# Performance work log

Measured on AMD Instinct MI355X. Metric: run time of the kernel, lower is better.

The kernel has to match this reference:

```python
import jax, jax.numpy as jnp
import numpy as np


def _conv1x1(x, w, b):
    # x: [B, Cin, H, W]; w: [Cout, Cin, 1, 1]; b: [Cout]
    y = jnp.einsum('bchw,oc->bohw', x, w[:, :, 0, 0])
    return y + b[None, :, None, None]


def setup_inputs() -> dict:
    key = jax.random.key(0)
    ks = jax.random.split(key, 9)
    B, C, H, W = 8, 256, 64, 64
    Cq = C // 4
    sc = 0.05
    return {
        'x': jax.random.normal(ks[0], (B, C, H, W), jnp.float32),
        'query_weight': jax.random.normal(ks[1], (Cq, C, 1, 1), jnp.float32) * sc,
        'query_bias': jax.random.normal(ks[2], (Cq,), jnp.float32) * sc,
        'key_weight': jax.random.normal(ks[3], (Cq, C, 1, 1), jnp.float32) * sc,
        'key_bias': jax.random.normal(ks[4], (Cq,), jnp.float32) * sc,
        'value_weight': jax.random.normal(ks[5], (C, C, 1, 1), jnp.float32) * sc,
        'value_bias': jax.random.normal(ks[6], (C,), jnp.float32) * sc,
        'gamma_weight': jax.random.normal(ks[7], (C, C, 1, 1), jnp.float32) * sc,
        'gamma_bias': jax.random.normal(ks[8], (C,), jnp.float32) * sc,
    }


def reference(x, query_weight, query_bias, key_weight, key_bias,
              value_weight, value_bias, gamma_weight, gamma_bias):
    B, C, H, W = x.shape
    N = H * W
    q = _conv1x1(x, query_weight, query_bias).reshape(B, -1, N)   # [B, Cq, N]
    k = _conv1x1(x, key_weight, key_bias).reshape(B, -1, N)       # [B, Cq, N]
    v = _conv1x1(x, value_weight, value_bias).reshape(B, C, N)    # [B, C, N]
    # energy[b, i, j] = sum_c q[b, c, i] * k[b, c, j]
    energy = jnp.einsum('bci,bcj->bij', q, k)                     # [B, N, N]
    energy = jax.nn.elu(energy) / N
    out = jnp.einsum('bcn,bnm->bcm', v, energy).reshape(B, C, H, W)
    return _conv1x1(out, gamma_weight, gamma_bias)
```

## Files before the change

### kernel.cpp

```cpp
#include <hip/hip_runtime.h>
#include <cmath>

#define BB 8
#define CC 256
#define CQ 64
#define NN 4096
constexpr float INV_N = 1.0f / 4096.0f;

typedef __attribute__((ext_vector_type(8))) short short8;
typedef __attribute__((ext_vector_type(4))) short short4v;
typedef __attribute__((ext_vector_type(4))) float float4v;

__device__ __forceinline__ short f2bf(float f) {
  union { float f; unsigned u; } x; x.f = f;
  unsigned r = x.u + 0x7fffu + ((x.u >> 16) & 1u);
  return (short)(r >> 16);
}

__global__ void wconv_kernel(const float* __restrict__ wq,
                             const float* __restrict__ wk,
                             const float* __restrict__ wv,
                             const float* __restrict__ wg,
                             short* __restrict__ wqb, short* __restrict__ wkb,
                             short* __restrict__ wvb, short* __restrict__ wgb) {
  const int t = blockIdx.x * 256 + threadIdx.x;
  const float* src;
  short* dst;
  int idx;
  if (t < 4096)        { src = wq; dst = wqb; idx = t; }
  else if (t < 8192)   { src = wk; dst = wkb; idx = t - 4096; }
  else if (t < 24576)  { src = wv; dst = wvb; idx = t - 8192; }
  else                 { src = wg; dst = wgb; idx = t - 24576; }
  const float4 v = *reinterpret_cast<const float4*>(&src[(size_t)idx * 4]);
  short4v o;
  o[0] = f2bf(v.x); o[1] = f2bf(v.y); o[2] = f2bf(v.z); o[3] = f2bf(v.w);
  *reinterpret_cast<short4v*>(&dst[(size_t)idx * 4]) = o;
}

__global__ __launch_bounds__(256, 2) void qkv_kernel(
    const float* __restrict__ X,
    const short* __restrict__ wqb, const float* __restrict__ bq,
    const short* __restrict__ wkb, const float* __restrict__ bk,
    const short* __restrict__ wvb, const float* __restrict__ bv,
    short* __restrict__ qt, short* __restrict__ kt, short* __restrict__ vbf) {
  __shared__ short xt[64 * 272];
  __shared__ short Os[64 * 72];
  const int tid = threadIdx.x;
  const int wid = tid >> 6;
  const int lane = tid & 63, quad = lane >> 4, l16 = lane & 15;
  const int b = blockIdx.x, n0 = blockIdx.y * 64;

#pragma unroll 4
  for (int p = 0; p < 16; ++p) {
    const int idx = p * 256 + tid;
    const int c = idx >> 4;
    const int n4 = (idx & 15) * 4;
    const float4 x4 = *reinterpret_cast<const float4*>(
        &X[((size_t)b * CC + c) * NN + n0 + n4]);
    xt[(n4 + 0) * 272 + c] = f2bf(x4.x);
    xt[(n4 + 1) * 272 + c] = f2bf(x4.y);
    xt[(n4 + 2) * 272 + c] = f2bf(x4.z);
    xt[(n4 + 3) * 272 + c] = f2bf(x4.w);
  }
  __syncthreads();

  for (int ch = 0; ch < 6; ++ch) {
    const short* W; const float* bias; int obase;
    if (ch == 0)      { W = wqb; bias = bq; obase = 0; }
    else if (ch == 1) { W = wkb; bias = bk; obase = 0; }
    else { W = wvb + (size_t)(ch - 2) * 64 * CC; bias = bv + (ch - 2) * 64; obase = (ch - 2) * 64; }

    float4v acc[4];
#pragma unroll
    for (int tm = 0; tm < 4; ++tm) acc[tm] = float4v{0.f, 0.f, 0.f, 0.f};

    const short* wrow = &W[(size_t)(wid * 16 + l16) * CC + quad * 8];
    short8 a_cur = *reinterpret_cast<const short8*>(wrow);
#pragma unroll
    for (int kk = 0; kk < 8; ++kk) {
      short8 a_nxt = a_cur;
      if (kk < 7) a_nxt = *reinterpret_cast<const short8*>(wrow + (kk + 1) * 32);
#pragma unroll
      for (int tm = 0; tm < 4; ++tm) {
        const short8 bfrag = *reinterpret_cast<const short8*>(
            &xt[(tm * 16 + l16) * 272 + kk * 32 + quad * 8]);
        acc[tm] = __builtin_amdgcn_mfma_f32_16x16x32_bf16(a_cur, bfrag, acc[tm], 0, 0, 0);
      }
      a_cur = a_nxt;
    }

    if (ch < 2) {
      short* dst = (ch == 0) ? qt : kt;
#pragma unroll
      for (int tm = 0; tm < 4; ++tm) {
        short4v pk;
#pragma unroll
        for (int r = 0; r < 4; ++r)
          pk[r] = f2bf(acc[tm][r] + bias[wid * 16 + quad * 4 + r]);
        *reinterpret_cast<short4v*>(
            &dst[((size_t)b * NN + n0 + tm * 16 + l16) * 64 + wid * 16 + quad * 4]) = pk;
      }
    } else {
      __syncthreads();
#pragma unroll
      for (int tm = 0; tm < 4; ++tm)
#pragma unroll
        for (int r = 0; r < 4; ++r)
          Os[(wid * 16 + quad * 4 + r) * 72 + tm * 16 + l16] =
              f2bf(acc[tm][r] + bias[wid * 16 + quad * 4 + r]);
      __syncthreads();
      const int o = tid >> 2, ng = (tid & 3) * 16;
      const short8 s0 = *reinterpret_cast<const short8*>(&Os[o * 72 + ng]);
      const short8 s1 = *reinterpret_cast<const short8*>(&Os[o * 72 + ng + 8]);
      short* vp = &vbf[((size_t)b * CC + obase + o) * NN + n0 + ng];
      *reinterpret_cast<short8*>(vp) = s0;
      *reinterpret_cast<short8*>(vp + 8) = s1;
    }
  }
}

__global__ __launch_bounds__(256, 2) void attn_kernel(
    const short* __restrict__ qt, const short* __restrict__ kt,
    const short* __restrict__ vbf, const short* __restrict__ wgb,
    const float* __restrict__ bg, float* __restrict__ out) {
  __shared__ short smem[16896];
  short* Es0 = smem;
  short* Es1 = smem + 4608;
  short* Outs = smem;

  const int tid = threadIdx.x;
  const int wid = tid >> 6;
  const int lane = tid & 63, quad = lane >> 4, l16 = lane & 15;
  const int b = blockIdx.x, m0 = blockIdx.y * 64;

  short8 bkf[4][2];
#pragma unroll
  for (int tm = 0; tm < 4; ++tm)
#pragma unroll
    for (int kk = 0; kk < 2; ++kk)
      bkf[tm][kk] = *reinterpret_cast<const short8*>(
          &kt[((size_t)b * NN + m0 + tm * 16 + l16) * 64 + kk * 32 + quad * 8]);

  const short* qrow = &qt[((size_t)b * NN + wid * 16 + l16) * 64 + quad * 8];
  const short* vrow[4];
#pragma unroll
  for (int tc = 0; tc < 4; ++tc)
    vrow[tc] = &vbf[((size_t)b * CC + wid * 64 + tc * 16 + l16) * NN + quad * 8];

  float4v acc[4][4];
#pragma unroll
  for (int i = 0; i < 4; ++i)
#pragma unroll
    for (int j = 0; j < 4; ++j) acc[i][j] = float4v{0.f, 0.f, 0.f, 0.f};

  short8 aq0 = *reinterpret_cast<const short8*>(qrow);
  short8 aq1 = *reinterpret_cast<const short8*>(qrow + 32);
  short8 av0[4][2], av1[4][2];
#pragma unroll
  for (int tc = 0; tc < 4; ++tc) {
    av0[tc][0] = *reinterpret_cast<const short8*>(vrow[tc]);
    av0[tc][1] = *reinterpret_cast<const short8*>(vrow[tc] + 32);
  }

  auto body = [&](int it, short8 (&avc)[4][2], short8 (&avn)[4][2]) {
    short* Esw = (it & 1) ? Es1 : Es0;
    const int nbn = (it + 1) * 64;

#pragma unroll
    for (int tc = 0; tc < 4; ++tc) {
      avn[tc][0] = *reinterpret_cast<const short8*>(vrow[tc] + nbn);
      avn[tc][1] = *reinterpret_cast<const short8*>(vrow[tc] + nbn + 32);
    }

    float4v s[4];
#pragma unroll
    for (int tm = 0; tm < 4; ++tm) {
      float4v t = {0.f, 0.f, 0.f, 0.f};
      t = __builtin_amdgcn_mfma_f32_16x16x32_bf16(aq0, bkf[tm][0], t, 0, 0, 0);
      t = __builtin_amdgcn_mfma_f32_16x16x32_bf16(aq1, bkf[tm][1], t, 0, 0, 0);
      s[tm] = t;
    }

    const short8 aq0n = *reinterpret_cast<const short8*>(qrow + (size_t)nbn * 64);
    const short8 aq1n = *reinterpret_cast<const short8*>(qrow + (size_t)nbn * 64 + 32);

#pragma unroll
    for (int tm = 0; tm < 4; ++tm) {
      short4v pk;
#pragma unroll
      for (int r = 0; r < 4; ++r) {
        float sv = s[tm][r];
        sv = (sv > 0.f) ? sv : (__expf(sv) - 1.f);
        pk[r] = f2bf(sv * INV_N);
      }
      *reinterpret_cast<short4v*>(
          &Esw[(tm * 16 + l16) * 72 + wid * 16 + quad * 4]) = pk;
    }
    __syncthreads();

#pragma unroll
    for (int tm = 0; tm < 4; ++tm) {
      const short8 be0 = *reinterpret_cast<const short8*>(
          &Esw[(tm * 16 + l16) * 72 + quad * 8]);
      const short8 be1 = *reinterpret_cast<const short8*>(
          &Esw[(tm * 16 + l16) * 72 + 32 + quad * 8]);
#pragma unroll
      for (int tc = 0; tc < 4; ++tc) {
        acc[tc][tm] = __builtin_amdgcn_mfma_f32_16x16x32_bf16(avc[tc][0], be0, acc[tc][tm], 0, 0, 0);
        acc[tc][tm] = __builtin_amdgcn_mfma_f32_16x16x32_bf16(avc[tc][1], be1, acc[tc][tm], 0, 0, 0);
      }
    }
    aq0 = aq0n; aq1 = aq1n;
  };

  for (int it = 0; it < 64; it += 2) {
    body(it, av0, av1);
    body(it + 1, av1, av0);
  }

  __syncthreads();
#pragma unroll
  for (int tc = 0; tc < 4; ++tc)
#pragma unroll
    for (int tm = 0; tm < 4; ++tm) {
      short4v pk;
#pragma unroll
      for (int r = 0; r < 4; ++r) pk[r] = f2bf(acc[tc][tm][r]);
      *reinterpret_cast<short4v*>(
          &Outs[(tm * 16 + l16) * 264 + wid * 64 + tc * 16 + quad * 4]) = pk;
    }
  __syncthreads();

#pragma unroll
  for (int i = 0; i < 4; ++i)
#pragma unroll
    for (int j = 0; j < 4; ++j) acc[i][j] = float4v{0.f, 0.f, 0.f, 0.f};

  for (int ks8 = 0; ks8 < 8; ++ks8) {
    short8 ag[4];
#pragma unroll
    for (int to = 0; to < 4; ++to)
      ag[to] = *reinterpret_cast<const short8*>(
          &wgb[(size_t)(wid * 64 + to * 16 + l16) * CC + ks8 * 32 + quad * 8]);
    short8 bo[4];
#pragma unroll
    for (int tm = 0; tm < 4; ++tm)
      bo[tm] = *reinterpret_cast<const short8*>(
          &Outs[(tm * 16 + l16) * 264 + ks8 * 32 + quad * 8]);
#pragma unroll
    for (int to = 0; to < 4; ++to)
#pragma unroll
      for (int tm = 0; tm < 4; ++tm)
        acc[to][tm] =
            __builtin_amdgcn_mfma_f32_16x16x32_bf16(ag[to], bo[tm], acc[to][tm], 0, 0, 0);
  }

#pragma unroll
  for (int to = 0; to < 4; ++to) {
#pragma unroll
    for (int r = 0; r < 4; ++r) {
      const int o = wid * 64 + to * 16 + quad * 4 + r;
      const float bgv = bg[o];
#pragma unroll
      for (int tm = 0; tm < 4; ++tm) {
        out[((size_t)b * CC + o) * NN + m0 + tm * 16 + l16] =
            acc[to][tm][r] + bgv;
      }
    }
  }
}

extern "C" void kernel_launch(void* const* d_in, const int* in_sizes, int n_in,
                              void* d_out, int out_size, void* d_ws,
                              size_t ws_size, hipStream_t stream) {
  const float* x  = (const float*)d_in[0];
  const float* wq = (const float*)d_in[1];
  const float* bq = (const float*)d_in[2];
  const float* wk = (const float*)d_in[3];
  const float* bk = (const float*)d_in[4];
  const float* wv = (const float*)d_in[5];
  const float* bv = (const float*)d_in[6];
  const float* wg = (const float*)d_in[7];
  const float* bg = (const float*)d_in[8];
  float* out = (float*)d_out;

  short* qt  = (short*)d_ws;
  short* kt  = qt + (size_t)BB * NN * CQ;
  short* vbf = kt + (size_t)BB * NN * CQ;
  short* wqb = vbf + (size_t)BB * CC * NN;
  short* wkb = wqb + (size_t)CQ * CC;
  short* wvb = wkb + (size_t)CQ * CC;
  short* wgb = wvb + (size_t)CC * CC;

  wconv_kernel<<<dim3(160), 256, 0, stream>>>(wq, wk, wv, wg, wqb, wkb, wvb, wgb);
  qkv_kernel<<<dim3(BB, NN / 64), 256, 0, stream>>>(x, wqb, bq, wkb, bk, wvb, bv,
                                                    qt, kt, vbf);
  attn_kernel<<<dim3(BB, NN / 64), 256, 0, stream>>>(qt, kt, vbf, wgb, bg, out);
}
```

Measured before the change: 271.2 us.

## Halve spatial tile to 32 in QKV and attention kernels, raise occupancy

After: 419.5 us. 54.7% more time.

```diff
diff --git a/kernel.cpp b/kernel.cpp
--- a/kernel.cpp
+++ b/kernel.cpp
@@ -37,24 +37,24 @@
   *reinterpret_cast<short4v*>(&dst[(size_t)idx * 4]) = o;
 }
 
-__global__ __launch_bounds__(256, 2) void qkv_kernel(
+__global__ __launch_bounds__(256, 4) void qkv_kernel(
     const float* __restrict__ X,
     const short* __restrict__ wqb, const float* __restrict__ bq,
     const short* __restrict__ wkb, const float* __restrict__ bk,
     const short* __restrict__ wvb, const float* __restrict__ bv,
     short* __restrict__ qt, short* __restrict__ kt, short* __restrict__ vbf) {
-  __shared__ short xt[64 * 272];
-  __shared__ short Os[64 * 72];
+  __shared__ short xt[32 * 272];
+  __shared__ short Os[64 * 40];
   const int tid = threadIdx.x;
   const int wid = tid >> 6;
   const int lane = tid & 63, quad = lane >> 4, l16 = lane & 15;
-  const int b = blockIdx.x, n0 = blockIdx.y * 64;
+  const int b = blockIdx.x, n0 = blockIdx.y * 32;
 
 #pragma unroll 4
-  for (int p = 0; p < 16; ++p) {
+  for (int p = 0; p < 8; ++p) {
     const int idx = p * 256 + tid;
-    const int c = idx >> 4;
-    const int n4 = (idx & 15) * 4;
+    const int c = idx >> 3;
+    const int n4 = (idx & 7) * 4;
     const float4 x4 = *reinterpret_cast<const float4*>(
         &X[((size_t)b * CC + c) * NN + n0 + n4]);
     xt[(n4 + 0) * 272 + c] = f2bf(x4.x);
@@ -70,9 +70,9 @@
     else if (ch == 1) { W = wkb; bias = bk; obase = 0; }
     else { W = wvb + (size_t)(ch - 2) * 64 * CC; bias = bv + (ch - 2) * 64; obase = (ch - 2) * 64; }
 
-    float4v acc[4];
-#pragma unroll
-    for (int tm = 0; tm < 4; ++tm) acc[tm] = float4v{0.f, 0.f, 0.f, 0.f};
+    float4v acc[2];
+#pragma unroll
+    for (int tm = 0; tm < 2; ++tm) acc[tm] = float4v{0.f, 0.f, 0.f, 0.f};
 
     const short* wrow = &W[(size_t)(wid * 16 + l16) * CC + quad * 8];
     short8 a_cur = *reinterpret_cast<const short8*>(wrow);
@@ -81,7 +81,7 @@
       short8 a_nxt = a_cur;
       if (kk < 7) a_nxt = *reinterpret_cast<const short8*>(wrow + (kk + 1) * 32);
 #pragma unroll
-      for (int tm = 0; tm < 4; ++tm) {
+      for (int tm = 0; tm < 2; ++tm) {
         const short8 bfrag = *reinterpret_cast<const short8*>(
             &xt[(tm * 16 + l16) * 272 + kk * 32 + quad * 8]);
         acc[tm] = __builtin_amdgcn_mfma_f32_16x16x32_bf16(a_cur, bfrag, acc[tm], 0, 0, 0);
@@ -92,7 +92,7 @@
     if (ch < 2) {
       short* dst = (ch == 0) ? qt : kt;
 #pragma unroll
-      for (int tm = 0; tm < 4; ++tm) {
+      for (int tm = 0; tm < 2; ++tm) {
         short4v pk;
 #pragma unroll
         for (int r = 0; r < 4; ++r)
@@ -103,95 +103,86 @@
     } else {
       __syncthreads();
 #pragma unroll
-      for (int tm = 0; tm < 4; ++tm)
+      for (int tm = 0; tm < 2; ++tm)
 #pragma unroll
         for (int r = 0; r < 4; ++r)
-          Os[(wid * 16 + quad * 4 + r) * 72 + tm * 16 + l16] =
+          Os[(wid * 16 + quad * 4 + r) * 40 + tm * 16 + l16] =
               f2bf(acc[tm][r] + bias[wid * 16 + quad * 4 + r]);
       __syncthreads();
-      const int o = tid >> 2, ng = (tid & 3) * 16;
-      const short8 s0 = *reinterpret_cast<const short8*>(&Os[o * 72 + ng]);
-      const short8 s1 = *reinterpret_cast<const short8*>(&Os[o * 72 + ng + 8]);
+      const int o = tid >> 2, ng = (tid & 3) * 8;
+      const short8 s0 = *reinterpret_cast<const short8*>(&Os[o * 40 + ng]);
       short* vp = &vbf[((size_t)b * CC + obase + o) * NN + n0 + ng];
       *reinterpret_cast<short8*>(vp) = s0;
-      *reinterpret_cast<short8*>(vp + 8) = s1;
-    }
-  }
-}
-
-__global__ __launch_bounds__(256, 2) void attn_kernel(
+    }
+  }
+}
+
+__global__ __launch_bounds__(256, 4) void attn_kernel(
     const short* __restrict__ qt, const short* __restrict__ kt,
     const short* __restrict__ vbf, const short* __restrict__ wgb,
     const float* __restrict__ bg, float* __restrict__ out) {
-  __shared__ short smem[16896];
+  __shared__ short smem[8448];
   short* Es0 = smem;
-  short* Es1 = smem + 4608;
+  short* Es1 = smem + 2304;
   short* Outs = smem;
 
   const int tid = threadIdx.x;
   const int wid = tid >> 6;
   const int lane = tid & 63, quad = lane >> 4, l16 = lane & 15;
-  const int b = blockIdx.x, m0 = blockIdx.y * 64;
-
-  short8 bkf[4][2];
-#pragma unroll
-  for (int tm = 0; tm < 4; ++tm)
+  const int b = blockIdx.x, m0 = blockIdx.y * 32;
+
+  short8 bkf[2][2];
+#pragma unroll
+  for (int tm = 0; tm < 2; ++tm)
 #pragma unroll
     for (int kk = 0; kk < 2; ++kk)
       bkf[tm][kk] = *reinterpret_cast<const short8*>(
           &kt[((size_t)b * NN + m0 + tm * 16 + l16) * 64 + kk * 32 + quad * 8]);
 
-  const short* qrow = &qt[((size_t)b * NN + wid * 16 + l16) * 64 + quad * 8];
-  const short* vrow[4];
-#pragma unroll
-  for (int tc = 0; tc < 4; ++tc)
-    vrow[tc] = &vbf[((size_t)b * CC + wid * 64 + tc * 16 + l16) * NN + quad * 8];
-
-  float4v acc[4][4];
+  const short* qp = &qt[((size_t)b * NN + wid * 16 + l16) * 64 + quad * 8];
+  const short* vp0 = &vbf[((size_t)b * CC + wid * 64 +  0 + l16) * NN + quad * 8];
+  const short* vp1 = &vbf[((size_t)b * CC + wid * 64 + 16 + l16) * NN + quad * 8];
+  const short* vp2 = &vbf[((size_t)b * CC + wid * 64 + 32 + l16) * NN + quad * 8];
+  const short* vp3 = &vbf[((size_t)b * CC + wid * 64 + 48 + l16) * NN + quad * 8];
+
+  float4v acc[4][2];
 #pragma unroll
   for (int i = 0; i < 4; ++i)
 #pragma unroll
-    for (int j = 0; j < 4; ++j) acc[i][j] = float4v{0.f, 0.f, 0.f, 0.f};
-
-  short8 aq0 = *reinterpret_cast<const short8*>(qrow);
-  short8 aq1 = *reinterpret_cast<const short8*>(qrow + 32);
-  short8 av0[4][2], av1[4][2];
-#pragma unroll
-  for (int tc = 0; tc < 4; ++tc) {
-    av0[tc][0] = *reinterpret_cast<const short8*>(vrow[tc]);
-    av0[tc][1] = *reinterpret_cast<const short8*>(vrow[tc] + 32);
-  }
-
-  auto body = [&](int it, short8 (&avc)[4][2], short8 (&avn)[4][2]) {
+    for (int j = 0; j < 2; ++j) acc[i][j] = float4v{0.f, 0.f, 0.f, 0.f};
+
+  for (int it = 0; it < 64; ++it) {
     short* Esw = (it & 1) ? Es1 : Es0;
-    const int nbn = (it + 1) * 64;
-
-#pragma unroll
-    for (int tc = 0; tc < 4; ++tc) {
-      avn[tc][0] = *reinterpret_cast<const short8*>(vrow[tc] + nbn);
-      avn[tc][1] = *reinterpret_cast<const short8*>(vrow[tc] + nbn + 32);
-    }
-
-    float4v s[4];
-#pragma unroll
-    for (int tm = 0; tm < 4; ++tm) {
+
+    short8 av[4][2];
+    av[0][0] = *reinterpret_cast<const short8*>(vp0);
+    av[0][1] = *reinterpret_cast<const short8*>(vp0 + 32);
+    av[1][0] = *reinterpret_cast<const short8*>(vp1);
+    av[1][1] = *reinterpret_cast<const short8*>(vp1 + 32);
+    av[2][0] = *reinterpret_cast<const short8*>(vp2);
+    av[2][1] = *reinterpret_cast<const short8*>(vp2 + 32);
+    av[3][0] = *reinterpret_cast<const short8*>(vp3);
+    av[3][1] = *reinterpret_cast<const short8*>(vp3 + 32);
+    const short8 aq0 = *reinterpret_cast<const short8*>(qp);
+    const short8 aq1 = *reinterpret_cast<const short8*>(qp + 32);
+
+    float4v s[2];
+#pragma unroll
+    for (int tm = 0; tm < 2; ++tm) {
       float4v t = {0.f, 0.f, 0.f, 0.f};
       t = __builtin_amdgcn_mfma_f32_16x16x32_bf16(aq0, bkf[tm][0], t, 0, 0, 0);
       t = __builtin_amdgcn_mfma_f32_16x16x32_bf16(aq1, bkf[tm][1], t, 0, 0, 0);
       s[tm] = t;
     }
 
-    const short8 aq0n = *reinterpret_cast<const short8*>(qrow + (size_t)nbn * 64);
-    const short8 aq1n = *reinterpret_cast<const short8*>(qrow + (size_t)nbn * 64 + 32);
-
-#pragma unroll
-    for (int tm = 0; tm < 4; ++tm) {
+#pragma unroll
+    for (int tm = 0; tm < 2; ++tm) {
       short4v pk;
 #pragma unroll
       for (int r = 0; r < 4; ++r) {
         float sv = s[tm][r];
         sv = (sv > 0.f) ? sv : (__expf(sv) - 1.f);
-        pk[r] = f2bf(sv * INV_N);
+        pk[r] = f2bf(sv);
       }
       *reinterpret_cast<short4v*>(
           &Esw[(tm * 16 + l16) * 72 + wid * 16 + quad * 4]) = pk;
@@ -199,33 +190,33 @@
     __syncthreads();
 
 #pragma unroll
-    for (int tm = 0; tm < 4; ++tm) {
+    for (int tm = 0; tm < 2; ++tm) {
       const short8 be0 = *reinterpret_cast<const short8*>(
           &Esw[(tm * 16 + l16) * 72 + quad * 8]);
       const short8 be1 = *reinterpret_cast<const short8*>(
           &Esw[(tm * 16 + l16) * 72 + 32 + quad * 8]);
-#pragma unroll
-      for (int tc = 0; tc < 4; ++tc) {
-        acc[tc][tm] = __builtin_amdgcn_mfma_f32_16x16x32_bf16(avc[tc][0], be0, acc[tc][tm], 0, 0, 0);
-        acc[tc][tm] = __builtin_amdgcn_mfma_f32_16x16x32_bf16(avc[tc][1], be1, acc[tc][tm], 0, 0, 0);
-      }
-    }
-    aq0 = aq0n; aq1 = aq1n;
-  };
-
-  for (int it = 0; it < 64; it += 2) {
-    body(it, av0, av1);
-    body(it + 1, av1, av0);
+      acc[0][tm] = __builtin_amdgcn_mfma_f32_16x16x32_bf16(av[0][0], be0, acc[0][tm], 0, 0, 0);
+      acc[0][tm] = __builtin_amdgcn_mfma_f32_16x16x32_bf16(av[0][1], be1, acc[0][tm], 0, 0, 0);
+      acc[1][tm] = __builtin_amdgcn_mfma_f32_16x16x32_bf16(av[1][0], be0, acc[1][tm], 0, 0, 0);
+      acc[1][tm] = __builtin_amdgcn_mfma_f32_16x16x32_bf16(av[1][1], be1, acc[1][tm], 0, 0, 0);
+      acc[2][tm] = __builtin_amdgcn_mfma_f32_16x16x32_bf16(av[2][0], be0, acc[2][tm], 0, 0, 0);
+      acc[2][tm] = __builtin_amdgcn_mfma_f32_16x16x32_bf16(av[2][1], be1, acc[2][tm], 0, 0, 0);
+      acc[3][tm] = __builtin_amdgcn_mfma_f32_16x16x32_bf16(av[3][0], be0, acc[3][tm], 0, 0, 0);
+      acc[3][tm] = __builtin_amdgcn_mfma_f32_16x16x32_bf16(av[3][1], be1, acc[3][tm], 0, 0, 0);
+    }
+
+    qp += 64 * 64;
+    vp0 += 64; vp1 += 64; vp2 += 64; vp3 += 64;
   }
 
   __syncthreads();
 #pragma unroll
   for (int tc = 0; tc < 4; ++tc)
 #pragma unroll
-    for (int tm = 0; tm < 4; ++tm) {
+    for (int tm = 0; tm < 2; ++tm) {
       short4v pk;
 #pragma unroll
-      for (int r = 0; r < 4; ++r) pk[r] = f2bf(acc[tc][tm][r]);
+      for (int r = 0; r < 4; ++r) pk[r] = f2bf(acc[tc][tm][r] * INV_N);
       *reinterpret_cast<short4v*>(
           &Outs[(tm * 16 + l16) * 264 + wid * 64 + tc * 16 + quad * 4]) = pk;
     }
@@ -234,7 +225,7 @@
 #pragma unroll
   for (int i = 0; i < 4; ++i)
 #pragma unroll
-    for (int j = 0; j < 4; ++j) acc[i][j] = float4v{0.f, 0.f, 0.f, 0.f};
+    for (int j = 0; j < 2; ++j) acc[i][j] = float4v{0.f, 0.f, 0.f, 0.f};
 
   for (int ks8 = 0; ks8 < 8; ++ks8) {
     short8 ag[4];
@@ -242,15 +233,15 @@
     for (int to = 0; to < 4; ++to)
       ag[to] = *reinterpret_cast<const short8*>(
           &wgb[(size_t)(wid * 64 + to * 16 + l16) * CC + ks8 * 32 + quad * 8]);
-    short8 bo[4];
-#pragma unroll
-    for (int tm = 0; tm < 4; ++tm)
+    short8 bo[2];
+#pragma unroll
+    for (int tm = 0; tm < 2; ++tm)
       bo[tm] = *reinterpret_cast<const short8*>(
           &Outs[(tm * 16 + l16) * 264 + ks8 * 32 + quad * 8]);
 #pragma unroll
     for (int to = 0; to < 4; ++to)
 #pragma unroll
-      for (int tm = 0; tm < 4; ++tm)
+      for (int tm = 0; tm < 2; ++tm)
         acc[to][tm] =
             __builtin_amdgcn_mfma_f32_16x16x32_bf16(ag[to], bo[tm], acc[to][tm], 0, 0, 0);
   }
@@ -262,7 +253,7 @@
       const int o = wid * 64 + to * 16 + quad * 4 + r;
       const float bgv = bg[o];
 #pragma unroll
-      for (int tm = 0; tm < 4; ++tm) {
+      for (int tm = 0; tm < 2; ++tm) {
         out[((size_t)b * CC + o) * NN + m0 + tm * 16 + l16] =
             acc[to][tm][r] + bgv;
       }
@@ -293,7 +284,7 @@
   short* wgb = wvb + (size_t)CC * CC;
 
   wconv_kernel<<<dim3(160), 256, 0, stream>>>(wq, wk, wv, wg, wqb, wkb, wvb, wgb);
-  qkv_kernel<<<dim3(BB, NN / 64), 256, 0, stream>>>(x, wqb, bq, wkb, bk, wvb, bv,
+  qkv_kernel<<<dim3(BB, NN / 32), 256, 0, stream>>>(x, wqb, bq, wkb, bk, wvb, bv,
                                                     qt, kt, vbf);
-  attn_kernel<<<dim3(BB, NN / 64), 256, 0, stream>>>(qt, kt, vbf, wgb, bg, out);
-}
+  attn_kernel<<<dim3(BB, NN / 32), 256, 0, stream>>>(qt, kt, vbf, wgb, bg, out);
+}
```

## Process two key blocks per sync in attention loop and batch-load inputs

Applied to the files above, without the earlier changes.

Measured after the change: 276.9 us. 2.1% more time.

```diff
diff --git a/kernel.cpp b/kernel.cpp
--- a/kernel.cpp
+++ b/kernel.cpp
@@ -50,17 +50,24 @@
   const int lane = tid & 63, quad = lane >> 4, l16 = lane & 15;
   const int b = blockIdx.x, n0 = blockIdx.y * 64;
 
-#pragma unroll 4
+  float4 xb[16];
+#pragma unroll
   for (int p = 0; p < 16; ++p) {
     const int idx = p * 256 + tid;
     const int c = idx >> 4;
     const int n4 = (idx & 15) * 4;
-    const float4 x4 = *reinterpret_cast<const float4*>(
+    xb[p] = *reinterpret_cast<const float4*>(
         &X[((size_t)b * CC + c) * NN + n0 + n4]);
-    xt[(n4 + 0) * 272 + c] = f2bf(x4.x);
-    xt[(n4 + 1) * 272 + c] = f2bf(x4.y);
-    xt[(n4 + 2) * 272 + c] = f2bf(x4.z);
-    xt[(n4 + 3) * 272 + c] = f2bf(x4.w);
+  }
+#pragma unroll
+  for (int p = 0; p < 16; ++p) {
+    const int idx = p * 256 + tid;
+    const int c = idx >> 4;
+    const int n4 = (idx & 15) * 4;
+    xt[(n4 + 0) * 272 + c] = f2bf(xb[p].x);
+    xt[(n4 + 1) * 272 + c] = f2bf(xb[p].y);
+    xt[(n4 + 2) * 272 + c] = f2bf(xb[p].z);
+    xt[(n4 + 3) * 272 + c] = f2bf(xb[p].w);
   }
   __syncthreads();
 
@@ -75,18 +82,19 @@
     for (int tm = 0; tm < 4; ++tm) acc[tm] = float4v{0.f, 0.f, 0.f, 0.f};
 
     const short* wrow = &W[(size_t)(wid * 16 + l16) * CC + quad * 8];
-    short8 a_cur = *reinterpret_cast<const short8*>(wrow);
+    short8 wf[8];
+#pragma unroll
+    for (int kk = 0; kk < 8; ++kk)
+      wf[kk] = *reinterpret_cast<const short8*>(wrow + kk * 32);
+
 #pragma unroll
     for (int kk = 0; kk < 8; ++kk) {
-      short8 a_nxt = a_cur;
-      if (kk < 7) a_nxt = *reinterpret_cast<const short8*>(wrow + (kk + 1) * 32);
 #pragma unroll
       for (int tm = 0; tm < 4; ++tm) {
         const short8 bfrag = *reinterpret_cast<const short8*>(
             &xt[(tm * 16 + l16) * 272 + kk * 32 + quad * 8]);
-        acc[tm] = __builtin_amdgcn_mfma_f32_16x16x32_bf16(a_cur, bfrag, acc[tm], 0, 0, 0);
-      }
-      a_cur = a_nxt;
+        acc[tm] = __builtin_amdgcn_mfma_f32_16x16x32_bf16(wf[kk], bfrag, acc[tm], 0, 0, 0);
+      }
     }
 
     if (ch < 2) {
@@ -123,9 +131,7 @@
     const short* __restrict__ qt, const short* __restrict__ kt,
     const short* __restrict__ vbf, const short* __restrict__ wgb,
     const float* __restrict__ bg, float* __restrict__ out) {
-  __shared__ short smem[16896];
-  short* Es0 = smem;
-  short* Es1 = smem + 4608;
+  __shared__ short smem[18432];
   short* Outs = smem;
 
   const int tid = threadIdx.x;
@@ -141,91 +147,116 @@
       bkf[tm][kk] = *reinterpret_cast<const short8*>(
           &kt[((size_t)b * NN + m0 + tm * 16 + l16) * 64 + kk * 32 + quad * 8]);
 
-  const short* qrow = &qt[((size_t)b * NN + wid * 16 + l16) * 64 + quad * 8];
-  const short* vrow[4];
+  const short* qp = &qt[((size_t)b * NN + wid * 16 + l16) * 64 + quad * 8];
+  const short* vp0 = &vbf[((size_t)b * CC + wid * 64 +  0 + l16) * NN + quad * 8];
+  const short* vp1 = &vbf[((size_t)b * CC + wid * 64 + 16 + l16) * NN + quad * 8];
+  const short* vp2 = &vbf[((size_t)b * CC + wid * 64 + 32 + l16) * NN + quad * 8];
+  const short* vp3 = &vbf[((size_t)b * CC + wid * 64 + 48 + l16) * NN + quad * 8];
+
+  float4v acc[4][4];
+#pragma unroll
+  for (int i = 0; i < 4; ++i)
+#pragma unroll
+    for (int j = 0; j < 4; ++j) acc[i][j] = float4v{0.f, 0.f, 0.f, 0.f};
+
+  for (int p = 0; p < 32; ++p) {
+    short* EA = smem + ((p & 1) ? 9216 : 0);
+    short* EB = smem + ((p & 1) ? 13824 : 4608);
+
+    const short8 aqA0 = *reinterpret_cast<const short8*>(qp);
+    const short8 aqA1 = *reinterpret_cast<const short8*>(qp + 32);
+    const short8 aqB0 = *reinterpret_cast<const short8*>(qp + 4096);
+    const short8 aqB1 = *reinterpret_cast<const short8*>(qp + 4096 + 32);
+    short8 avA[4][2];
+    avA[0][0] = *reinterpret_cast<const short8*>(vp0);
+    avA[0][1] = *reinterpret_cast<const short8*>(vp0 + 32);
+    avA[1][0] = *reinterpret_cast<const short8*>(vp1);
+    avA[1][1] = *reinterpret_cast<const short8*>(vp1 + 32);
+    avA[2][0] = *reinterpret_cast<const short8*>(vp2);
+    avA[2][1] = *reinterpret_cast<const short8*>(vp2 + 32);
+    avA[3][0] = *reinterpret_cast<const short8*>(vp3);
+    avA[3][1] = *reinterpret_cast<const short8*>(vp3 + 32);
+
+#pragma unroll
+    for (int tm = 0; tm < 4; ++tm) {
+      float4v t = {0.f, 0.f, 0.f, 0.f};
+      t = __builtin_amdgcn_mfma_f32_16x16x32_bf16(aqA0, bkf[tm][0], t, 0, 0, 0);
+      t = __builtin_amdgcn_mfma_f32_16x16x32_bf16(aqA1, bkf[tm][1], t, 0, 0, 0);
+      short4v pk;
+#pragma unroll
+      for (int r = 0; r < 4; ++r) {
+        float sv = t[r];
+        sv = (sv > 0.f) ? sv : (__expf(sv) - 1.f);
+        pk[r] = f2bf(sv);
+      }
+      *reinterpret_cast<short4v*>(
+          &EA[(tm * 16 + l16) * 72 + wid * 16 + quad * 4]) = pk;
+    }
+
+#pragma unroll
+    for (int tm = 0; tm < 4; ++tm) {
+      float4v t = {0.f, 0.f, 0.f, 0.f};
+      t = __builtin_amdgcn_mfma_f32_16x16x32_bf16(aqB0, bkf[tm][0], t, 0, 0, 0);
+      t = __builtin_amdgcn_mfma_f32_16x16x32_bf16(aqB1, bkf[tm][1], t, 0, 0, 0);
+      short4v pk;
+#pragma unroll
+      for (int r = 0; r < 4; ++r) {
+        float sv = t[r];
+        sv = (sv > 0.f) ? sv : (__expf(sv) - 1.f);
+        pk[r] = f2bf(sv);
+      }
+      *reinterpret_cast<short4v*>(
+          &EB[(tm * 16 + l16) * 72 + wid * 16 + quad * 4]) = pk;
+    }
+    __syncthreads();
+
+    short8 avB[4][2];
+    avB[0][0] = *reinterpret_cast<const short8*>(vp0 + 64);
+    avB[0][1] = *reinterpret_cast<const short8*>(vp0 + 96);
+    avB[1][0] = *reinterpret_cast<const short8*>(vp1 + 64);
+    avB[1][1] = *reinterpret_cast<const short8*>(vp1 + 96);
+    avB[2][0] = *reinterpret_cast<const short8*>(vp2 + 64);
+    avB[2][1] = *reinterpret_cast<const short8*>(vp2 + 96);
+    avB[3][0] = *reinterpret_cast<const short8*>(vp3 + 64);
+    avB[3][1] = *reinterpret_cast<const short8*>(vp3 + 96);
+
+#pragma unroll
+    for (int tm = 0; tm < 4; ++tm) {
+      const short8 be0 = *reinterpret_cast<const short8*>(
+          &EA[(tm * 16 + l16) * 72 + quad * 8]);
+      const short8 be1 = *reinterpret_cast<const short8*>(
+          &EA[(tm * 16 + l16) * 72 + 32 + quad * 8]);
+#pragma unroll
+      for (int tc = 0; tc < 4; ++tc) {
+        acc[tc][tm] = __builtin_amdgcn_mfma_f32_16x16x32_bf16(avA[tc][0], be0, acc[tc][tm], 0, 0, 0);
+        acc[tc][tm] = __builtin_amdgcn_mfma_f32_16x16x32_bf16(avA[tc][1], be1, acc[tc][tm], 0, 0, 0);
+      }
+    }
+#pragma unroll
+    for (int tm = 0; tm < 4; ++tm) {
+      const short8 be0 = *reinterpret_cast<const short8*>(
+          &EB[(tm * 16 + l16) * 72 + quad * 8]);
+      const short8 be1 = *reinterpret_cast<const short8*>(
+          &EB[(tm * 16 + l16) * 72 + 32 + quad * 8]);
+#pragma unroll
+      for (int tc = 0; tc < 4; ++tc) {
+        acc[tc][tm] = __builtin_amdgcn_mfma_f32_16x16x32_bf16(avB[tc][0], be0, acc[tc][tm], 0, 0, 0);
+        acc[tc][tm] = __builtin_amdgcn_mfma_f32_16x16x32_bf16(avB[tc][1], be1, acc[tc][tm], 0, 0, 0);
+      }
+    }
+
+    qp += 2 * 64 * 64;
+    vp0 += 128; vp1 += 128; vp2 += 128; vp3 += 128;
+  }
+
+  __syncthreads();
 #pragma unroll
   for (int tc = 0; tc < 4; ++tc)
-    vrow[tc] = &vbf[((size_t)b * CC + wid * 64 + tc * 16 + l16) * NN + quad * 8];
-
-  float4v acc[4][4];
-#pragma unroll
-  for (int i = 0; i < 4; ++i)
-#pragma unroll
-    for (int j = 0; j < 4; ++j) acc[i][j] = float4v{0.f, 0.f, 0.f, 0.f};
-
-  short8 aq0 = *reinterpret_cast<const short8*>(qrow);
-  short8 aq1 = *reinterpret_cast<const short8*>(qrow + 32);
-  short8 av0[4][2], av1[4][2];
-#pragma unroll
-  for (int tc = 0; tc < 4; ++tc) {
-    av0[tc][0] = *reinterpret_cast<const short8*>(vrow[tc]);
-    av0[tc][1] = *reinterpret_cast<const short8*>(vrow[tc] + 32);
-  }
-
-  auto body = [&](int it, short8 (&avc)[4][2], short8 (&avn)[4][2]) {
-    short* Esw = (it & 1) ? Es1 : Es0;
-    const int nbn = (it + 1) * 64;
-
-#pragma unroll
-    for (int tc = 0; tc < 4; ++tc) {
-      avn[tc][0] = *reinterpret_cast<const short8*>(vrow[tc] + nbn);
-      avn[tc][1] = *reinterpret_cast<const short8*>(vrow[tc] + nbn + 32);
-    }
-
-    float4v s[4];
-#pragma unroll
-    for (int tm = 0; tm < 4; ++tm) {
-      float4v t = {0.f, 0.f, 0.f, 0.f};
-      t = __builtin_amdgcn_mfma_f32_16x16x32_bf16(aq0, bkf[tm][0], t, 0, 0, 0);
-      t = __builtin_amdgcn_mfma_f32_16x16x32_bf16(aq1, bkf[tm][1], t, 0, 0, 0);
-      s[tm] = t;
-    }
-
-    const short8 aq0n = *reinterpret_cast<const short8*>(qrow + (size_t)nbn * 64);
-    const short8 aq1n = *reinterpret_cast<const short8*>(qrow + (size_t)nbn * 64 + 32);
-
 #pragma unroll
     for (int tm = 0; tm < 4; ++tm) {
       short4v pk;
 #pragma unroll
-      for (int r = 0; r < 4; ++r) {
-        float sv = s[tm][r];
-        sv = (sv > 0.f) ? sv : (__expf(sv) - 1.f);
-        pk[r] = f2bf(sv * INV_N);
-      }
-      *reinterpret_cast<short4v*>(
-          &Esw[(tm * 16 + l16) * 72 + wid * 16 + quad * 4]) = pk;
-    }
-    __syncthreads();
-
-#pragma unroll
-    for (int tm = 0; tm < 4; ++tm) {
-      const short8 be0 = *reinterpret_cast<const short8*>(
-          &Esw[(tm * 16 + l16) * 72 + quad * 8]);
-      const short8 be1 = *reinterpret_cast<const short8*>(
-          &Esw[(tm * 16 + l16) * 72 + 32 + quad * 8]);
-#pragma unroll
-      for (int tc = 0; tc < 4; ++tc) {
-        acc[tc][tm] = __builtin_amdgcn_mfma_f32_16x16x32_bf16(avc[tc][0], be0, acc[tc][tm], 0, 0, 0);
-        acc[tc][tm] = __builtin_amdgcn_mfma_f32_16x16x32_bf16(avc[tc][1], be1, acc[tc][tm], 0, 0, 0);
-      }
-    }
-    aq0 = aq0n; aq1 = aq1n;
-  };
-
-  for (int it = 0; it < 64; it += 2) {
-    body(it, av0, av1);
-    body(it + 1, av1, av0);
-  }
-
-  __syncthreads();
-#pragma unroll
-  for (int tc = 0; tc < 4; ++tc)
-#pragma unroll
-    for (int tm = 0; tm < 4; ++tm) {
-      short4v pk;
-#pragma unroll
-      for (int r = 0; r < 4; ++r) pk[r] = f2bf(acc[tc][tm][r]);
+      for (int r = 0; r < 4; ++r) pk[r] = f2bf(acc[tc][tm][r] * INV_N);
       *reinterpret_cast<short4v*>(
           &Outs[(tm * 16 + l16) * 264 + wid * 64 + tc * 16 + quad * 4]) = pk;
     }
```

## Software-pipeline attention energy with PV matmul and cache operands in registers

Applied to the files above, without the earlier changes.

Result: no change. 272.3 us (+0.4%).

```diff
diff --git a/kernel.cpp b/kernel.cpp
--- a/kernel.cpp
+++ b/kernel.cpp
@@ -43,26 +43,44 @@
     const short* __restrict__ wkb, const float* __restrict__ bk,
     const short* __restrict__ wvb, const float* __restrict__ bv,
     short* __restrict__ qt, short* __restrict__ kt, short* __restrict__ vbf) {
-  __shared__ short xt[64 * 272];
-  __shared__ short Os[64 * 72];
+  __shared__ short xt[64 * 264];
   const int tid = threadIdx.x;
   const int wid = tid >> 6;
   const int lane = tid & 63, quad = lane >> 4, l16 = lane & 15;
   const int b = blockIdx.x, n0 = blockIdx.y * 64;
 
-#pragma unroll 4
+  float4 xb[16];
+#pragma unroll
   for (int p = 0; p < 16; ++p) {
     const int idx = p * 256 + tid;
     const int c = idx >> 4;
     const int n4 = (idx & 15) * 4;
-    const float4 x4 = *reinterpret_cast<const float4*>(
+    xb[p] = *reinterpret_cast<const float4*>(
         &X[((size_t)b * CC + c) * NN + n0 + n4]);
-    xt[(n4 + 0) * 272 + c] = f2bf(x4.x);
-    xt[(n4 + 1) * 272 + c] = f2bf(x4.y);
-    xt[(n4 + 2) * 272 + c] = f2bf(x4.z);
-    xt[(n4 + 3) * 272 + c] = f2bf(x4.w);
+  }
+#pragma unroll
+  for (int p = 0; p < 16; ++p) {
+    const int idx = p * 256 + tid;
+    const int c = idx >> 4;
+    const int n4 = (idx & 15) * 4;
+    xt[(n4 + 0) * 264 + c] = f2bf(xb[p].x);
+    xt[(n4 + 1) * 264 + c] = f2bf(xb[p].y);
+    xt[(n4 + 2) * 264 + c] = f2bf(xb[p].z);
+    xt[(n4 + 3) * 264 + c] = f2bf(xb[p].w);
   }
   __syncthreads();
+
+  short8 bfr[8][4];
+#pragma unroll
+  for (int kk = 0; kk < 8; ++kk)
+#pragma unroll
+    for (int tm = 0; tm < 4; ++tm)
+      bfr[kk][tm] = *reinterpret_cast<const short8*>(
+          &xt[(tm * 16 + l16) * 264 + kk * 32 + quad * 8]);
+  __syncthreads();
+
+  short* Os0 = xt;
+  short* Os1 = xt + 4608;
 
   for (int ch = 0; ch < 6; ++ch) {
     const short* W; const float* bias; int obase;
@@ -70,24 +88,20 @@
     else if (ch == 1) { W = wkb; bias = bk; obase = 0; }
     else { W = wvb + (size_t)(ch - 2) * 64 * CC; bias = bv + (ch - 2) * 64; obase = (ch - 2) * 64; }
 
+    const short* wrow = &W[(size_t)(wid * 16 + l16) * CC + quad * 8];
+    short8 wf[8];
+#pragma unroll
+    for (int kk = 0; kk < 8; ++kk)
+      wf[kk] = *reinterpret_cast<const short8*>(wrow + kk * 32);
+
     float4v acc[4];
 #pragma unroll
     for (int tm = 0; tm < 4; ++tm) acc[tm] = float4v{0.f, 0.f, 0.f, 0.f};
-
-    const short* wrow = &W[(size_t)(wid * 16 + l16) * CC + quad * 8];
-    short8 a_cur = *reinterpret_cast<const short8*>(wrow);
-#pragma unroll
-    for (int kk = 0; kk < 8; ++kk) {
-      short8 a_nxt = a_cur;
-      if (kk < 7) a_nxt = *reinterpret_cast<const short8*>(wrow + (kk + 1) * 32);
-#pragma unroll
-      for (int tm = 0; tm < 4; ++tm) {
-        const short8 bfrag = *reinterpret_cast<const short8*>(
-            &xt[(tm * 16 + l16) * 272 + kk * 32 + quad * 8]);
-        acc[tm] = __builtin_amdgcn_mfma_f32_16x16x32_bf16(a_cur, bfrag, acc[tm], 0, 0, 0);
-      }
-      a_cur = a_nxt;
-    }
+#pragma unroll
+    for (int kk = 0; kk < 8; ++kk)
+#pragma unroll
+      for (int tm = 0; tm < 4; ++tm)
+        acc[tm] = __builtin_amdgcn_mfma_f32_16x16x32_bf16(wf[kk], bfr[kk][tm], acc[tm], 0, 0, 0);
 
     if (ch < 2) {
       short* dst = (ch == 0) ? qt : kt;
@@ -101,7 +115,7 @@
             &dst[((size_t)b * NN + n0 + tm * 16 + l16) * 64 + wid * 16 + quad * 4]) = pk;
       }
     } else {
-      __syncthreads();
+      short* Os = (ch & 1) ? Os1 : Os0;
 #pragma unroll
       for (int tm = 0; tm < 4; ++tm)
 #pragma unroll
@@ -141,7 +155,7 @@
       bkf[tm][kk] = *reinterpret_cast<const short8*>(
           &kt[((size_t)b * NN + m0 + tm * 16 + l16) * 64 + kk * 32 + quad * 8]);
 
-  const short* qrow = &qt[((size_t)b * NN + wid * 16 + l16) * 64 + quad * 8];
+  const short* qp = &qt[((size_t)b * NN + wid * 16 + l16) * 64 + quad * 8];
   const short* vrow[4];
 #pragma unroll
   for (int tc = 0; tc < 4; ++tc)
@@ -153,79 +167,103 @@
 #pragma unroll
     for (int j = 0; j < 4; ++j) acc[i][j] = float4v{0.f, 0.f, 0.f, 0.f};
 
-  short8 aq0 = *reinterpret_cast<const short8*>(qrow);
-  short8 aq1 = *reinterpret_cast<const short8*>(qrow + 32);
-  short8 av0[4][2], av1[4][2];
+  short8 avA[4][2], avB[4][2];
 #pragma unroll
   for (int tc = 0; tc < 4; ++tc) {
-    av0[tc][0] = *reinterpret_cast<const short8*>(vrow[tc]);
-    av0[tc][1] = *reinterpret_cast<const short8*>(vrow[tc] + 32);
-  }
-
-  auto body = [&](int it, short8 (&avc)[4][2], short8 (&avn)[4][2]) {
-    short* Esw = (it & 1) ? Es1 : Es0;
-    const int nbn = (it + 1) * 64;
-
-#pragma unroll
-    for (int tc = 0; tc < 4; ++tc) {
-      avn[tc][0] = *reinterpret_cast<const short8*>(vrow[tc] + nbn);
-      avn[tc][1] = *reinterpret_cast<const short8*>(vrow[tc] + nbn + 32);
-    }
-
-    float4v s[4];
+    avA[tc][0] = *reinterpret_cast<const short8*>(vrow[tc]);
+    avA[tc][1] = *reinterpret_cast<const short8*>(vrow[tc] + 32);
+  }
+  short8 aqA0 = *reinterpret_cast<const short8*>(qp + (size_t)1 * 4096);
+  short8 aqA1 = *reinterpret_cast<const short8*>(qp + (size_t)1 * 4096 + 32);
+  short8 aqB0, aqB1;
+  {
+    const short8 aq0 = *reinterpret_cast<const short8*>(qp);
+    const short8 aq1 = *reinterpret_cast<const short8*>(qp + 32);
 #pragma unroll
     for (int tm = 0; tm < 4; ++tm) {
       float4v t = {0.f, 0.f, 0.f, 0.f};
       t = __builtin_amdgcn_mfma_f32_16x16x32_bf16(aq0, bkf[tm][0], t, 0, 0, 0);
       t = __builtin_amdgcn_mfma_f32_16x16x32_bf16(aq1, bkf[tm][1], t, 0, 0, 0);
-      s[tm] = t;
-    }
-
-    const short8 aq0n = *reinterpret_cast<const short8*>(qrow + (size_t)nbn * 64);
-    const short8 aq1n = *reinterpret_cast<const short8*>(qrow + (size_t)nbn * 64 + 32);
-
-#pragma unroll
-    for (int tm = 0; tm < 4; ++tm) {
       short4v pk;
 #pragma unroll
       for (int r = 0; r < 4; ++r) {
-        float sv = s[tm][r];
+        float sv = t[r];
         sv = (sv > 0.f) ? sv : (__expf(sv) - 1.f);
-        pk[r] = f2bf(sv * INV_N);
+        pk[r] = f2bf(sv);
       }
       *reinterpret_cast<short4v*>(
-          &Esw[(tm * 16 + l16) * 72 + wid * 16 + quad * 4]) = pk;
-    }
-    __syncthreads();
+          &Es0[(tm * 16 + l16) * 72 + wid * 16 + quad * 4]) = pk;
+    }
+  }
+  __syncthreads();
+
+  auto seg = [&](int it, short8 (&avc)[4][2], short8 (&avn)[4][2],
+                 short8& aqc0, short8& aqc1, short8& aqn0, short8& aqn1) {
+    const int nb1 = (it + 1) * 64;
+#pragma unroll
+    for (int tc = 0; tc < 4; ++tc) {
+      avn[tc][0] = *reinterpret_cast<const short8*>(vrow[tc] + nb1);
+      avn[tc][1] = *reinterpret_cast<const short8*>(vrow[tc] + nb1 + 32);
+    }
+    aqn0 = *reinterpret_cast<const short8*>(qp + (size_t)(it + 2) * 4096);
+    aqn1 = *reinterpret_cast<const short8*>(qp + (size_t)(it + 2) * 4096 + 32);
+
+    short* Esr = (it & 1) ? Es1 : Es0;
+    short* Esw = (it & 1) ? Es0 : Es1;
+
+    float4v s[4];
+    if (it < 63) {
+#pragma unroll
+      for (int tm = 0; tm < 4; ++tm) {
+        float4v t = {0.f, 0.f, 0.f, 0.f};
+        t = __builtin_amdgcn_mfma_f32_16x16x32_bf16(aqc0, bkf[tm][0], t, 0, 0, 0);
+        t = __builtin_amdgcn_mfma_f32_16x16x32_bf16(aqc1, bkf[tm][1], t, 0, 0, 0);
+        s[tm] = t;
+      }
+    }
 
 #pragma unroll
     for (int tm = 0; tm < 4; ++tm) {
       const short8 be0 = *reinterpret_cast<const short8*>(
-          &Esw[(tm * 16 + l16) * 72 + quad * 8]);
+          &Esr[(tm * 16 + l16) * 72 + quad * 8]);
       const short8 be1 = *reinterpret_cast<const short8*>(
-          &Esw[(tm * 16 + l16) * 72 + 32 + quad * 8]);
+          &Esr[(tm * 16 + l16) * 72 + 32 + quad * 8]);
 #pragma unroll
       for (int tc = 0; tc < 4; ++tc) {
         acc[tc][tm] = __builtin_amdgcn_mfma_f32_16x16x32_bf16(avc[tc][0], be0, acc[tc][tm], 0, 0, 0);
         acc[tc][tm] = __builtin_amdgcn_mfma_f32_16x16x32_bf16(avc[tc][1], be1, acc[tc][tm], 0, 0, 0);
       }
     }
-    aq0 = aq0n; aq1 = aq1n;
+
+    if (it < 63) {
+#pragma unroll
+      for (int tm = 0; tm < 4; ++tm) {
+        short4v pk;
+#pragma unroll
+        for (int r = 0; r < 4; ++r) {
+          float sv = s[tm][r];
+          sv = (sv > 0.f) ? sv : (__expf(sv) - 1.f);
+          pk[r] = f2bf(sv);
+        }
+        *reinterpret_cast<short4v*>(
+            &Esw[(tm * 16 + l16) * 72 + wid * 16 + quad * 4]) = pk;
+      }
+    }
+    __syncthreads();
   };
 
   for (int it = 0; it < 64; it += 2) {
-    body(it, av0, av1);
-    body(it + 1, av1, av0);
-  }
-
-  __syncthreads();
+    seg(it,     avA, avB, aqA0, aqA1, aqB0, aqB1);
+    seg(it + 1, avB, avA, aqB0, aqB1, aqA0, aqA1);
+  }
+
 #pragma unroll
   for (int tc = 0; tc < 4; ++tc)
 #pragma unroll
     for (int tm = 0; tm < 4; ++tm) {
       short4v pk;
 #pragma unroll
-      for (int r = 0; r < 4; ++r) pk[r] = f2bf(acc[tc][tm][r]);
+      for (int r = 0; r < 4; ++r) pk[r] = f2bf(acc[tc][tm][r] * INV_N);
       *reinterpret_cast<short4v*>(
           &Outs[(tm * 16 + l16) * 264 + wid * 64 + tc * 16 + quad * 4]) = pk;
     }
```
